# Optimization experiments

Hardware: AMD Instinct MI355X
Metric: run time of the kernel (lower is better)

Reference implementation:

```python
import jax, jax.numpy as jnp
import numpy as np

EMBED_DIM = 1024
NUM_HEADS = 16
HEAD_DIM = EMBED_DIM // NUM_HEADS
# Source divides by scale = head_dim**-0.5, i.e. multiplies logits by sqrt(head_dim).
INV_SCALE = float(HEAD_DIM) ** 0.5


def setup_inputs() -> dict:
    key = jax.random.key(0)
    ks = jax.random.split(key, 9)
    E = EMBED_DIM
    s = 1.0 / np.sqrt(E)
    x = jax.random.normal(ks[0], (2, 2048, E), dtype=jnp.float32)
    Wq = jax.random.uniform(ks[1], (E, E), jnp.float32, -s, s)
    bq = jax.random.uniform(ks[2], (E,), jnp.float32, -s, s)
    Wk = jax.random.uniform(ks[3], (E, E), jnp.float32, -s, s)
    bk = jax.random.uniform(ks[4], (E,), jnp.float32, -s, s)
    Wv = jax.random.uniform(ks[5], (E, E), jnp.float32, -s, s)
    bv = jax.random.uniform(ks[6], (E,), jnp.float32, -s, s)
    Wo = jax.random.uniform(ks[7], (E, E), jnp.float32, -s, s)
    bo = jax.random.uniform(ks[8], (E,), jnp.float32, -s, s)
    return {"x": x, "Wq": Wq, "bq": bq, "Wk": Wk, "bk": bk,
            "Wv": Wv, "bv": bv, "Wo": Wo, "bo": bo}


def reference(x, Wq, bq, Wk, bk, Wv, bv, Wo, bo):
    B, N, C = x.shape
    H, D = NUM_HEADS, HEAD_DIM
    # nn.Linear: y = x @ W.T + b
    q = (x @ Wq.T + bq).reshape(B, N, H, D).transpose(0, 2, 1, 3)  # [B,H,N,D]
    k = (x @ Wk.T + bk).reshape(B, N, H, D).transpose(0, 2, 1, 3)
    v = (x @ Wv.T + bv).reshape(B, N, H, D).transpose(0, 2, 1, 3)
    # Faithful to source: logits = QK^T / (head_dim**-0.5) = QK^T * sqrt(head_dim)
    logits = jnp.einsum('bhnd,bhmd->bhnm', q, k) * INV_SCALE  # [B,H,N,N]
    attn = jax.nn.softmax(logits, axis=-1)
    h = jnp.einsum('bhnm,bhmd->bhnd', attn, v)  # [B,H,N,D]
    concat_h = h.transpose(0, 2, 1, 3).reshape(B, N, C)
    return concat_h @ Wo.T + bo
```

## Files before the change

kernel.cpp:

```cpp
#include <hip/hip_runtime.h>
#include <math.h>

#define B_ 2
#define N_ 2048
#define E_ 1024
#define H_ 16
#define D_ 64

typedef unsigned short US;
typedef _Float16 h16x8 __attribute__((ext_vector_type(8)));
typedef _Float16 h16x4 __attribute__((ext_vector_type(4)));
typedef __fp16 fp16x2 __attribute__((ext_vector_type(2)));
typedef float f32x4 __attribute__((ext_vector_type(4)));
#define MFMA16F(a,b,c)  __builtin_amdgcn_mfma_f32_16x16x32_f16(a,b,c,0,0,0)
#define MFMA161(a,b,c)  __builtin_amdgcn_mfma_f32_16x16x16f16(a,b,c,0,0,0)
#define SCL  11.5415603828f

union HU { _Float16 h; US u; };
__device__ __forceinline__ US f2h(float f){ HU x; x.h = (_Float16)f; return x.u; }
__device__ __forceinline__ unsigned pkrtz(float a, float b){
  union { fp16x2 h; unsigned u; } x;
  x.h = __builtin_amdgcn_cvt_pkrtz(a, b);
  return x.u;
}

union U8 { US u[8]; uint4 v; };
union U4 { US u[4]; uint2 v; };
union UPA { unsigned u[2]; h16x4 h; };

__device__ __forceinline__ void glds16(const US* g, US* l){
  __builtin_amdgcn_global_load_lds(
    (const __attribute__((address_space(1))) unsigned int*)(const void*)g,
    (__attribute__((address_space(3))) unsigned int*)(void*)l, 16, 0, 0);
}

__global__ __launch_bounds__(256) void conv_all(
    const float* __restrict__ x,
    const float* __restrict__ w0, const float* __restrict__ w1,
    const float* __restrict__ w2, const float* __restrict__ w3,
    US* __restrict__ xh, US* __restrict__ Wall)
{
  const int id = blockIdx.x;
  const float* s; US* d; size_t off;
  if (id < 2048) { s = x; d = xh; off = (size_t)id*2048; }
  else {
    int j = id - 2048, wsel = j>>9;
    off = (size_t)(j&511)*2048;
    s = (wsel==0)?w0:(wsel==1)?w1:(wsel==2)?w2:w3;
    d = Wall + (size_t)wsel*1048576;
  }
  size_t i = off + (size_t)threadIdx.x*8;
  float f[8];
  *(float4*)&f[0] = *(const float4*)&s[i];
  *(float4*)&f[4] = *(const float4*)&s[i+4];
  U8 h;
  #pragma unroll
  for (int j=0;j<8;++j) h.u[j] = f2h(f[j]);
  *(uint4*)&d[i] = h.v;
}

__global__ __launch_bounds__(256,3) void qkv_gemm(
    const US* __restrict__ A, const US* __restrict__ Wall,
    const float* __restrict__ bq, const float* __restrict__ bk, const float* __restrict__ bv,
    US* __restrict__ Qf, US* __restrict__ Kf, US* __restrict__ Vtb)
{
  __shared__ __align__(16) US sA[128*32];
  __shared__ __align__(16) US sW[128*32];
  const int z = blockIdx.z;
  const US* W = Wall + (size_t)z*1048576;
  const float* bias = (z==0)?bq:(z==1)?bk:bv;

  const int t = threadIdx.x;
  const int w = t>>6, lane = t&63;
  const int q = lane>>4, c = lane&15;
  const int mq = (w>>1)*64, nq = (w&1)*64;
  const int gm0 = blockIdx.y*128, gn0 = blockIdx.x*128;
  const int r16 = lane>>2, seg = lane&3;

  f32x4 acc[4][4] = {};
  for (int kb = 0; kb < 1024; kb += 32) {
    #pragma unroll
    for (int p=0;p<2;++p){
      int rb = (w*2+p)*16;
      glds16(&A[(size_t)(gm0 + rb + r16)*1024 + kb + seg*8], &sA[rb*32]);
      glds16(&W[(size_t)(gn0 + rb + r16)*1024 + kb + seg*8], &sW[rb*32]);
    }
    __syncthreads();
    h16x8 af[4], wf[4];
    #pragma unroll
    for (int rt=0;rt<4;++rt) af[rt] = *(const h16x8*)&sA[(mq+rt*16+c)*32 + q*8];
    #pragma unroll
    for (int ct=0;ct<4;++ct) wf[ct] = *(const h16x8*)&sW[(nq+ct*16+c)*32 + q*8];
    #pragma unroll
    for (int rt=0;rt<4;++rt)
      #pragma unroll
      for (int ct=0;ct<4;++ct)
        acc[rt][ct] = MFMA16F(af[rt], wf[ct], acc[rt][ct]);
    __syncthreads();
  }
  #pragma unroll
  for (int rt=0;rt<4;++rt)
  #pragma unroll
  for (int ct=0;ct<4;++ct) {
    int col = gn0 + nq + ct*16 + c;
    float bv_ = bias[col];
    int rowb = gm0 + mq + rt*16 + q*4;
    int hh = col>>6, d = col & 63;
    if (z==2) {
      int b = rowb>>11, n = rowb & (N_-1);
      U4 pk;
      #pragma unroll
      for (int r=0;r<4;++r) pk.u[r] = f2h(acc[rt][ct][r] + bv_);
      *(uint2*)&Vtb[((size_t)(b*H_+hh)*D_ + d)*N_ + n] = pk.v;
    } else {
      US* dst = (z==0) ? Qf : Kf;
      #pragma unroll
      for (int r=0;r<4;++r) {
        int row = rowb + r;
        float v = acc[rt][ct][r] + bv_;
        if (z==0) v *= SCL;
        int b = row>>11, n = row & (N_-1);
        dst[((size_t)(b*H_+hh)*N_+n)*D_ + d] = f2h(v);
      }
    }
  }
}

__global__ __launch_bounds__(256,4) void o_gemm(
    const US* __restrict__ A, const US* __restrict__ W,
    const float* __restrict__ bias, float* __restrict__ out)
{
  __shared__ __align__(16) US sA[128*32];
  __shared__ __align__(16) US sW[64*32];
  const int t = threadIdx.x;
  const int w = t>>6, lane = t&63;
  const int q = lane>>4, c = lane&15;
  const int gm0 = blockIdx.y*128, gn0 = blockIdx.x*64;
  const int r16 = lane>>2, seg = lane&3;

  f32x4 acc[2][4] = {};
  for (int kb = 0; kb < 1024; kb += 32) {
    glds16(&A[(size_t)(gm0 + w*32      + r16)*1024 + kb + seg*8], &sA[(w*32)*32]);
    glds16(&A[(size_t)(gm0 + w*32 + 16 + r16)*1024 + kb + seg*8], &sA[(w*32+16)*32]);
    glds16(&W[(size_t)(gn0 + w*16      + r16)*1024 + kb + seg*8], &sW[(w*16)*32]);
    __syncthreads();
    h16x8 af0 = *(const h16x8*)&sA[(w*32+c)*32 + q*8];
    h16x8 af1 = *(const h16x8*)&sA[(w*32+16+c)*32 + q*8];
    #pragma unroll
    for (int ct=0; ct<4; ++ct){
      h16x8 wf = *(const h16x8*)&sW[(ct*16+c)*32 + q*8];
      acc[0][ct] = MFMA16F(af0, wf, acc[0][ct]);
      acc[1][ct] = MFMA16F(af1, wf, acc[1][ct]);
    }
    __syncthreads();
  }
  #pragma unroll
  for (int rt=0; rt<2; ++rt)
  #pragma unroll
  for (int ct=0; ct<4; ++ct) {
    int col = gn0 + ct*16 + c;
    float bv_ = bias[col];
    int rowb = gm0 + w*32 + rt*16 + q*4;
    #pragma unroll
    for (int r=0;r<4;++r)
      out[(size_t)(rowb+r)*1024 + col] = acc[rt][ct][r] + bv_;
  }
}

#define KSTR2 72
#define VSTR  136
__global__ __launch_bounds__(512,4) void attn(
    const US* __restrict__ Qf, const US* __restrict__ Kf, const US* __restrict__ Vt,
    US* __restrict__ Hout)
{
  __shared__ __align__(16) US sK [2][128*KSTR2];
  __shared__ __align__(16) US sVt[2][64*VSTR];
  const int t = threadIdx.x;
  const int w = t>>6, lane = t&63, q = lane>>4, c = lane&15;
  const int id = blockIdx.x;
  const int bh = ((id & 7) << 2) | ((id >> 3) & 3);
  const int n0 = (id >> 5) * 128;
  const US* Kp = Kf + (size_t)bh * (N_*D_);
  const US* Vp = Vt + (size_t)bh * (D_*N_);

  const size_t qoff = (size_t)bh*(N_*D_) + (size_t)(n0 + w*16 + c)*D_;
  h16x8 qb0 = *(const h16x8*)&Qf[qoff + q*8];
  h16x8 qb1 = *(const h16x8*)&Qf[qoff + 32 + q*8];
  h16x4 vones;
  #pragma unroll
  for (int j=0;j<4;++j) vones[j] = (_Float16)1.0f;

  float mi = -INFINITY;
  f32x4 o[5] = {};

  const int kr = t>>3, kc8 = (t&7)*8;
  const int vr = t>>4, vc8 = (t&15)*8;

  #pragma unroll
  for (int p=0;p<2;++p){
    int r = p*64 + kr;
    *(uint4*)&sK[0][r*KSTR2 + kc8] = *(const uint4*)&Kp[(size_t)r*D_ + kc8];
  }
  #pragma unroll
  for (int p=0;p<2;++p){
    int r = p*32 + vr;
    *(uint4*)&sVt[0][r*VSTR + vc8] = *(const uint4*)&Vp[(size_t)r*N_ + vc8];
  }
  __syncthreads();

  for (int mt=0; mt<16; ++mt) {
    const int cur = mt&1;
    uint4 kreg[2], vreg[2];
    if (mt < 15){
      const int m1 = (mt+1)*128;
      #pragma unroll
      for (int p=0;p<2;++p)
        kreg[p] = *(const uint4*)&Kp[(size_t)(m1 + p*64 + kr)*D_ + kc8];
      #pragma unroll
      for (int p=0;p<2;++p)
        vreg[p] = *(const uint4*)&Vp[(size_t)(p*32 + vr)*N_ + m1 + vc8];
    }

    f32x4 s[8];
    __builtin_amdgcn_s_setprio(1);
    #pragma unroll
    for (int f=0; f<8; ++f){
      h16x8 k0 = *(const h16x8*)&sK[cur][(f*16+c)*KSTR2 + q*8];
      h16x8 k1 = *(const h16x8*)&sK[cur][(f*16+c)*KSTR2 + 32 + q*8];
      f32x4 sv = {};
      sv = MFMA16F(k0, qb0, sv);
      sv = MFMA16F(k1, qb1, sv);
      s[f] = sv;
    }
    __builtin_amdgcn_s_setprio(0);

    f32x4 vm = s[0];
    #pragma unroll
    for (int f=1; f<8; ++f){
      vm[0]=fmaxf(vm[0],s[f][0]); vm[1]=fmaxf(vm[1],s[f][1]);
      vm[2]=fmaxf(vm[2],s[f][2]); vm[3]=fmaxf(vm[3],s[f][3]);
    }
    float v = fmaxf(fmaxf(vm[0],vm[1]), fmaxf(vm[2],vm[3]));
    v = fmaxf(v, __shfl_xor(v, 16));
    v = fmaxf(v, __shfl_xor(v, 32));
    float mnew = fmaxf(mi, v);
    if (!__all(v <= mi)) {
      float alpha = exp2f(mi-mnew);
      float ar[4];
      #pragma unroll
      for (int r=0; r<4; ++r) ar[r] = __shfl(alpha, q*4+r);
      #pragma unroll
      for (int dt=0; dt<5; ++dt){
        o[dt][0]*=ar[0]; o[dt][1]*=ar[1]; o[dt][2]*=ar[2]; o[dt][3]*=ar[3];
      }
    }
    mi = mnew;
    #pragma unroll
    for (int f=0; f<8; ++f){
      float p0 = exp2f(s[f][0]-mnew);
      float p1 = exp2f(s[f][1]-mnew);
      float p2 = exp2f(s[f][2]-mnew);
      float p3 = exp2f(s[f][3]-mnew);
      UPA pa;
      pa.u[0] = pkrtz(p0, p1);
      pa.u[1] = pkrtz(p2, p3);
      h16x4 pah = pa.h;
      __builtin_amdgcn_s_setprio(1);
      #pragma unroll
      for (int dt=0; dt<4; ++dt){
        h16x4 vf = *(const h16x4*)&sVt[cur][(dt*16+c)*VSTR + f*16 + q*4];
        o[dt] = MFMA161(pah, vf, o[dt]);
      }
      o[4] = MFMA161(pah, vones, o[4]);
      __builtin_amdgcn_s_setprio(0);
    }

    if (mt < 15){
      #pragma unroll
      for (int p=0;p<2;++p)
        *(uint4*)&sK[cur^1][(p*64+kr)*KSTR2 + kc8] = kreg[p];
      #pragma unroll
      for (int p=0;p<2;++p)
        *(uint4*)&sVt[cur^1][(p*32+vr)*VSTR + vc8] = vreg[p];
    }
    __syncthreads();
  }

  const int b = bh>>4, hh = bh&15;
  float ir[4];
  #pragma unroll
  for (int r=0; r<4; ++r) ir[r] = 1.0f / o[4][r];
  #pragma unroll
  for (int dt=0; dt<4; ++dt){
    #pragma unroll
    for (int r=0; r<4; ++r){
      int n = n0 + w*16 + q*4 + r;
      int d = dt*16 + c;
      Hout[((size_t)(b*N_+n)*H_+hh)*D_ + d] = f2h(o[dt][r] * ir[r]);
    }
  }
}

extern "C" void kernel_launch(void* const* d_in, const int* in_sizes, int n_in,
                              void* d_out, int out_size, void* d_ws, size_t ws_size,
                              hipStream_t stream)
{
  const float* x  = (const float*)d_in[0];
  const float* Wq = (const float*)d_in[1];
  const float* bq = (const float*)d_in[2];
  const float* Wk = (const float*)d_in[3];
  const float* bk = (const float*)d_in[4];
  const float* Wv = (const float*)d_in[5];
  const float* bv = (const float*)d_in[6];
  const float* Wo = (const float*)d_in[7];
  const float* bo = (const float*)d_in[8];
  US* ws  = (US*)d_ws;
  const size_t M1 = 1048576;
  US* xh   = ws;
  US* Wall = ws + 4*M1;
  US* Qf   = ws + 8*M1;
  US* Kf   = ws + 12*M1;
  US* Vtb  = ws + 16*M1;
  US* Hf   = ws + 20*M1;

  conv_all<<<4096, 256, 0, stream>>>(x, Wq, Wk, Wv, Wo, xh, Wall);
  qkv_gemm<<<dim3(8,32,3), 256, 0, stream>>>(xh, Wall, bq, bk, bv, Qf, Kf, Vtb);
  attn<<<512, 512, 0, stream>>>(Qf, Kf, Vtb, Hf);
  o_gemm<<<dim3(16,32), 256, 0, stream>>>(Hf, Wall + 3*M1, bo, (float*)d_out);
}
```

Before: 209.9 us.

## Shrink o_gemm tiles to 64x64 and add lazy softmax rescaling

The output projection GEMM now uses 64x64 block tiles with a 2x2 warp layout, twice as many blocks, and launch bounds allowing 8 blocks per CU. This gives more parallelism and occupancy for a 4096x1024 output, at the cost of more repeated operand loads. The attention kernel restructures its max reduction into a shallower tree and skips rescaling the accumulators unless the new running max exceeds the old one by more than 8 (in log2 units). This saves exp and multiply work per tile, but unnormalized probabilities can reach up to 2^8, which raises fp16 overflow risk in the P·V accumulation.

```diff
diff --git a/kernel.cpp b/kernel.cpp
--- a/kernel.cpp
+++ b/kernel.cpp
@@ -126,41 +126,43 @@
   }
 }
 
-__global__ __launch_bounds__(256,4) void o_gemm(
+__global__ __launch_bounds__(256,8) void o_gemm(
     const US* __restrict__ A, const US* __restrict__ W,
     const float* __restrict__ bias, float* __restrict__ out)
 {
-  __shared__ __align__(16) US sA[128*32];
+  __shared__ __align__(16) US sA[64*32];
   __shared__ __align__(16) US sW[64*32];
   const int t = threadIdx.x;
   const int w = t>>6, lane = t&63;
   const int q = lane>>4, c = lane&15;
-  const int gm0 = blockIdx.y*128, gn0 = blockIdx.x*64;
-  const int r16 = lane>>2, seg = lane&3;
-
-  f32x4 acc[2][4] = {};
+  const int wr = (w>>1)*32, wc = (w&1)*32;
+  const int gm0 = blockIdx.y*64, gn0 = blockIdx.x*64;
+  const int r4 = lane>>2, seg = lane&3;
+
+  f32x4 acc[2][2] = {};
   for (int kb = 0; kb < 1024; kb += 32) {
-    glds16(&A[(size_t)(gm0 + w*32      + r16)*1024 + kb + seg*8], &sA[(w*32)*32]);
-    glds16(&A[(size_t)(gm0 + w*32 + 16 + r16)*1024 + kb + seg*8], &sA[(w*32+16)*32]);
-    glds16(&W[(size_t)(gn0 + w*16      + r16)*1024 + kb + seg*8], &sW[(w*16)*32]);
-    __syncthreads();
-    h16x8 af0 = *(const h16x8*)&sA[(w*32+c)*32 + q*8];
-    h16x8 af1 = *(const h16x8*)&sA[(w*32+16+c)*32 + q*8];
-    #pragma unroll
-    for (int ct=0; ct<4; ++ct){
-      h16x8 wf = *(const h16x8*)&sW[(ct*16+c)*32 + q*8];
-      acc[0][ct] = MFMA16F(af0, wf, acc[0][ct]);
-      acc[1][ct] = MFMA16F(af1, wf, acc[1][ct]);
-    }
+    glds16(&A[(size_t)(gm0 + w*16 + r4)*1024 + kb + seg*8], &sA[(w*16)*32]);
+    glds16(&W[(size_t)(gn0 + w*16 + r4)*1024 + kb + seg*8], &sW[(w*16)*32]);
+    __syncthreads();
+    h16x8 af[2], wf[2];
+    #pragma unroll
+    for (int rt=0;rt<2;++rt) af[rt] = *(const h16x8*)&sA[(wr+rt*16+c)*32 + q*8];
+    #pragma unroll
+    for (int ct=0;ct<2;++ct) wf[ct] = *(const h16x8*)&sW[(wc+ct*16+c)*32 + q*8];
+    #pragma unroll
+    for (int rt=0;rt<2;++rt)
+      #pragma unroll
+      for (int ct=0;ct<2;++ct)
+        acc[rt][ct] = MFMA16F(af[rt], wf[ct], acc[rt][ct]);
     __syncthreads();
   }
   #pragma unroll
   for (int rt=0; rt<2; ++rt)
   #pragma unroll
-  for (int ct=0; ct<4; ++ct) {
-    int col = gn0 + ct*16 + c;
+  for (int ct=0; ct<2; ++ct) {
+    int col = gn0 + wc + ct*16 + c;
     float bv_ = bias[col];
-    int rowb = gm0 + w*32 + rt*16 + q*4;
+    int rowb = gm0 + wr + rt*16 + q*4;
     #pragma unroll
     for (int r=0;r<4;++r)
       out[(size_t)(rowb+r)*1024 + col] = acc[rt][ct][r] + bv_;
@@ -234,18 +236,20 @@
     }
     __builtin_amdgcn_s_setprio(0);
 
-    f32x4 vm = s[0];
-    #pragma unroll
-    for (int f=1; f<8; ++f){
-      vm[0]=fmaxf(vm[0],s[f][0]); vm[1]=fmaxf(vm[1],s[f][1]);
-      vm[2]=fmaxf(vm[2],s[f][2]); vm[3]=fmaxf(vm[3],s[f][3]);
-    }
-    float v = fmaxf(fmaxf(vm[0],vm[1]), fmaxf(vm[2],vm[3]));
+    f32x4 t1;
+    #pragma unroll
+    for (int j=0;j<4;++j){
+      float a = fmaxf(fmaxf(s[0][j],s[1][j]),s[2][j]);
+      float b = fmaxf(fmaxf(s[3][j],s[4][j]),s[5][j]);
+      float d = fmaxf(fmaxf(s[6][j],s[7][j]),a);
+      t1[j] = fmaxf(b,d);
+    }
+    float v = fmaxf(fmaxf(t1[0],t1[1]), fmaxf(t1[2],t1[3]));
     v = fmaxf(v, __shfl_xor(v, 16));
     v = fmaxf(v, __shfl_xor(v, 32));
-    float mnew = fmaxf(mi, v);
-    if (!__all(v <= mi)) {
-      float alpha = exp2f(mi-mnew);
+    if (!__all(v <= mi + 8.0f)) {
+      float mnew = fmaxf(mi, v);
+      float alpha = exp2f(mi - mnew);
       float ar[4];
       #pragma unroll
       for (int r=0; r<4; ++r) ar[r] = __shfl(alpha, q*4+r);
@@ -253,14 +257,14 @@
       for (int dt=0; dt<5; ++dt){
         o[dt][0]*=ar[0]; o[dt][1]*=ar[1]; o[dt][2]*=ar[2]; o[dt][3]*=ar[3];
       }
-    }
-    mi = mnew;
+      mi = mnew;
+    }
     #pragma unroll
     for (int f=0; f<8; ++f){
-      float p0 = exp2f(s[f][0]-mnew);
-      float p1 = exp2f(s[f][1]-mnew);
-      float p2 = exp2f(s[f][2]-mnew);
-      float p3 = exp2f(s[f][3]-mnew);
+      float p0 = exp2f(s[f][0]-mi);
+      float p1 = exp2f(s[f][1]-mi);
+      float p2 = exp2f(s[f][2]-mi);
+      float p3 = exp2f(s[f][3]-mi);
       UPA pa;
       pa.u[0] = pkrtz(p0, p1);
       pa.u[1] = pkrtz(p2, p3);
@@ -326,5 +330,5 @@
   conv_all<<<4096, 256, 0, stream>>>(x, Wq, Wk, Wv, Wo, xh, Wall);
   qkv_gemm<<<dim3(8,32,3), 256, 0, stream>>>(xh, Wall, bq, bk, bv, Qf, Kf, Vtb);
   attn<<<512, 512, 0, stream>>>(Qf, Kf, Vtb, Hf);
-  o_gemm<<<dim3(16,32), 256, 0, stream>>>(Hf, Wall + 3*M1, bo, (float*)d_out);
-}
+  o_gemm<<<dim3(16,64), 256, 0, stream>>>(Hf, Wall + 3*M1, bo, (float*)d_out);
+}
```

Measured after the change: 206.2 us (median of 3 runs). Within noise of the previous version (-1.8%).
